# Kernel tuning notes

Hardware: AMD Instinct MI355X
Metric: run time of the kernel (lower is better)

The kernel has to match this reference:

```python
import jax, jax.numpy as jnp
import numpy as np

B, L, H, E, V = 32, 1024, 1024, 512, 8192

def setup_inputs() -> dict:
    key = jax.random.key(0)
    k1, k2, k3, k4 = jax.random.split(key, 4)
    x = jax.random.randint(k1, (B, L), 0, V)
    hidden = jnp.zeros((B, H), dtype=jnp.float32)  # equivalent to hidden=None path
    embedding = jax.random.normal(k2, (V, E), dtype=jnp.float32)
    W_h = jax.random.normal(k3, (E + H, H), dtype=jnp.float32) * 0.01
    b_h = jnp.zeros((H,), dtype=jnp.float32)
    W_o = jax.random.normal(k4, (H, V), dtype=jnp.float32) * 0.01
    b_o = jnp.zeros((V,), dtype=jnp.float32)
    return {"x": x, "hidden": hidden, "embedding": embedding,
            "W_h": W_h, "b_h": b_h, "W_o": W_o, "b_o": b_o}

def reference(x, hidden, embedding, W_h, b_h, W_o, b_o):
    # x: [B, L] int; hidden: [B, H]
    x_embed = embedding[x]                       # [B, L, E]
    x_tl = jnp.swapaxes(x_embed, 0, 1)           # [L, B, E] time-major

    def step(h, x_t):
        # concat + matmul + bias + tanh, one timestep
        combined = jnp.concatenate([x_t, h], axis=1)   # [B, E+H]
        h_new = jnp.tanh(combined @ W_h + b_h)         # [B, H]
        return h_new, h_new

    final_hidden, outs = jax.lax.scan(step, hidden, x_tl)  # outs: [L, B, H]
    output = jnp.swapaxes(outs, 0, 1)                       # [B, L, H]
    logits = output @ W_o + b_o                             # [B, L, V]
    return logits, final_hidden
```

## Files before the change

### kernel.cpp

```cpp
#include <hip/hip_runtime.h>
#include <hip/hip_bf16.h>

typedef unsigned short u16;
typedef unsigned int   u32;
typedef unsigned long long u64;
typedef __attribute__((ext_vector_type(8))) __bf16 bf16x8;
typedef __attribute__((ext_vector_type(4))) float   f32x4;

#define GLOAD16(gp, lp) __builtin_amdgcn_global_load_lds( \
    (__attribute__((address_space(1))) void*)(gp),        \
    (__attribute__((address_space(3))) void*)(lp), 16, 0, 0)

static __device__ __forceinline__ u16 f2bf(float f) {
  __bf16 b = (__bf16)f;
  return __builtin_bit_cast(u16, b);
}
static __device__ __forceinline__ f32x4 mfma16(bf16x8 a, bf16x8 b, f32x4 c) {
  return __builtin_amdgcn_mfma_f32_16x16x32_bf16(a, b, c, 0, 0, 0);
}


__global__ __launch_bounds__(256) void k_cvt_emb(const float* __restrict__ s,
                                                 u16* __restrict__ d) {
  int i = (blockIdx.x * 256 + threadIdx.x) * 4;
  float4 v = *(const float4*)(s + i);
  d[i] = f2bf(v.x); d[i+1] = f2bf(v.y); d[i+2] = f2bf(v.z); d[i+3] = f2bf(v.w);
}

__global__ __launch_bounds__(256) void k_tr_wh(const float* __restrict__ Wh,
                                               u16* __restrict__ WhxT,
                                               u16* __restrict__ WhhT) {
  __shared__ float tile[32][33];
  int bx = blockIdx.x & 31;
  int be = blockIdx.x >> 5;
  int tx = threadIdx.x & 31, ty = threadIdx.x >> 5;
  #pragma unroll
  for (int s = 0; s < 32; s += 8)
    tile[ty + s][tx] = Wh[(size_t)(be*32 + ty + s) * 1024 + bx*32 + tx];
  __syncthreads();
  #pragma unroll
  for (int s = 0; s < 32; s += 8) {
    int e = be*32 + tx;
    int j = bx*32 + ty + s;
    u16 v = f2bf(tile[tx][ty + s]);
    if (e < 512) WhxT[(size_t)j * 512 + e] = v;
    else         WhhT[(size_t)j * 1024 + (e - 512)] = v;
  }
}

__global__ __launch_bounds__(256) void k_tr_wo(const float* __restrict__ Wo,
                                               u16* __restrict__ WoT) {
  __shared__ float tile[32][33];
  int bx = blockIdx.x & 255;
  int by = blockIdx.x >> 8;
  int tx = threadIdx.x & 31, ty = threadIdx.x >> 5;
  #pragma unroll
  for (int s = 0; s < 32; s += 8)
    tile[ty + s][tx] = Wo[(size_t)(by*32 + ty + s) * 8192 + bx*32 + tx];
  __syncthreads();
  #pragma unroll
  for (int s = 0; s < 32; s += 8)
    WoT[(size_t)(bx*32 + ty + s) * 1024 + by*32 + tx] = f2bf(tile[tx][ty + s]);
}

__global__ __launch_bounds__(256) void k_init(const float* __restrict__ hid,
                                              u16* __restrict__ ring,
                                              unsigned* __restrict__ flags) {
  int i = blockIdx.x * 256 + threadIdx.x;
  ring[i] = f2bf(hid[i]);
  if (blockIdx.x < 8) flags[i] = 0;
}

__global__ __launch_bounds__(256) void k_xpart(const int* __restrict__ xq,
                                               const u16* __restrict__ embB,
                                               const u16* __restrict__ WhxT,
                                               const float* __restrict__ bh,
                                               float* __restrict__ xpart) {
  __shared__ __align__(16) u16 As[128 * 32];
  __shared__ __align__(16) u16 Bs[128 * 32];
  __shared__ int sx[128];
  int bid = blockIdx.x;
  int cpx = gridDim.x >> 3;
  int swz = (bid & 7) * cpx + (bid >> 3);
  int tm = (swz >> 3) * 128, tn = (swz & 7) * 128;
  int tid = threadIdx.x, lane = tid & 63, w = tid >> 6;
  int wm = (w >> 1) * 64, wn = (w & 1) * 64;
  if (tid < 128) sx[tid] = xq[tm + tid];
  __syncthreads();
  int r0 = tid >> 2, sub = tid & 3;
  const u16* ga0 = embB + (size_t)sx[r0] * 512 + sub * 8;
  const u16* ga1 = embB + (size_t)sx[64 + r0] * 512 + sub * 8;
  const u16* gb0 = WhxT + (size_t)(tn + r0) * 512 + sub * 8;
  const u16* gb1 = WhxT + (size_t)(tn + 64 + r0) * 512 + sub * 8;
  f32x4 acc[4][4] = {};
  int rl = lane & 15, kb = (lane >> 4) * 8;
  for (int kt = 0; kt < 16; ++kt) {
    int k0 = kt * 32;
    __syncthreads();
    GLOAD16(ga0 + k0, As + w * 512);
    GLOAD16(ga1 + k0, As + 2048 + w * 512);
    GLOAD16(gb0 + k0, Bs + w * 512);
    GLOAD16(gb1 + k0, Bs + 2048 + w * 512);
    __syncthreads();
    bf16x8 af[4], bf[4];
    #pragma unroll
    for (int mi = 0; mi < 4; mi++) af[mi] = *(const bf16x8*)&As[(wm + mi*16 + rl) * 32 + kb];
    #pragma unroll
    for (int ni = 0; ni < 4; ni++) bf[ni] = *(const bf16x8*)&Bs[(wn + ni*16 + rl) * 32 + kb];
    #pragma unroll
    for (int mi = 0; mi < 4; mi++)
      #pragma unroll
      for (int ni = 0; ni < 4; ni++)
        acc[mi][ni] = mfma16(af[mi], bf[ni], acc[mi][ni]);
  }
  int rq = (lane >> 4) << 2;
  #pragma unroll
  for (int ni = 0; ni < 4; ni++) {
    int col = tn + wn + ni*16 + rl;
    float bias = bh[col];
    #pragma unroll
    for (int mi = 0; mi < 4; mi++) {
      int row = tm + wm + mi*16 + rq;
      #pragma unroll
      for (int r = 0; r < 4; r++)
        xpart[(size_t)(row + r) * 1024 + col] = acc[mi][ni][r] + bias;
    }
  }
}

__global__ __launch_bounds__(256, 2) void k_fused(const u16* __restrict__ WhhT,
                                                  const float* __restrict__ xpart,
                                                  u16* __restrict__ ring,
                                                  float* __restrict__ hfinal,
                                                  unsigned* flags,
                                                  const u16* __restrict__ WoT,
                                                  const float* __restrict__ bo,
                                                  float* __restrict__ C) {
  __shared__ __align__(16) u16 smem[8192];
  __shared__ int sq;
  const int tid = threadIdx.x, lane = tid & 63, w = tid >> 6;

  if (blockIdx.x < 64) {
    float* psh = (float*)smem;
    int bid = blockIdx.x;
    int jbase = bid * 16;
    const int rl = lane & 15;
    const int kbase = w * 256 + ((lane >> 4) << 3);
    bf16x8 Wreg[8];
    #pragma unroll
    for (int ki = 0; ki < 8; ++ki)
      Wreg[ki] = *(const bf16x8*)&WhhT[(size_t)(jbase + rl) * 1024 + kbase + ki * 32];
    const bool red = (tid < 128);
    int b = 0, jq = 0, mi = 0, lsrc = 0, rg = 0;
    float4 xpre = make_float4(0.f, 0.f, 0.f, 0.f);
    if (red) {
      b = tid >> 2; jq = (tid & 3) << 2;
      mi = b >> 4;
      int bb = b & 15;
      lsrc = (bb >> 2) << 4;
      rg = bb & 3;
      xpre = *(const float4*)&xpart[(size_t)(b * 1024 + 0) * 1024 + jbase + jq];
    }
    for (int t = 0; t < 1024; ++t) {
      const u16* hprev = ring + (size_t)t * 32768;
      bf16x8 ha[16];
      #pragma unroll
      for (int ki = 0; ki < 8; ++ki) {
        int k = kbase + ki * 32;
        ha[ki*2 + 0] = *(const bf16x8*)&hprev[(size_t)rl * 1024 + k];
        ha[ki*2 + 1] = *(const bf16x8*)&hprev[(size_t)(16 + rl) * 1024 + k];
      }
      f32x4 acc0 = {0.f, 0.f, 0.f, 0.f}, acc1 = {0.f, 0.f, 0.f, 0.f};
      #pragma unroll
      for (int ki = 0; ki < 8; ++ki) {
        acc0 = mfma16(ha[ki*2 + 0], Wreg[ki], acc0);
        acc1 = mfma16(ha[ki*2 + 1], Wreg[ki], acc1);
      }
      *(f32x4*)&psh[((w * 2 + 0) * 64 + lane) * 4] = acc0;
      *(f32x4*)&psh[((w * 2 + 1) * 64 + lane) * 4] = acc1;
      __syncthreads();
      if (red) {
        float s0 = 0.f, s1 = 0.f, s2 = 0.f, s3 = 0.f;
        #pragma unroll
        for (int ww = 0; ww < 4; ++ww) {
          const float* pp = &psh[((ww * 2 + mi) * 64) * 4];
          s0 += pp[(lsrc + jq + 0) * 4 + rg];
          s1 += pp[(lsrc + jq + 1) * 4 + rg];
          s2 += pp[(lsrc + jq + 2) * 4 + rg];
          s3 += pp[(lsrc + jq + 3) * 4 + rg];
        }
        float v0 = tanhf(s0 + xpre.x);
        float v1 = tanhf(s1 + xpre.y);
        float v2 = tanhf(s2 + xpre.z);
        float v3 = tanhf(s3 + xpre.w);
        u32 lo = (u32)f2bf(v0) | ((u32)f2bf(v1) << 16);
        u32 hi = (u32)f2bf(v2) | ((u32)f2bf(v3) << 16);
        u64 hv = (u64)lo | ((u64)hi << 32);
        __hip_atomic_store((u64*)(ring + (size_t)(t + 1) * 32768 + b * 1024 + jbase + jq),
                           hv, __ATOMIC_RELAXED, __HIP_MEMORY_SCOPE_AGENT);
        if (t == 1023)
          *(float4*)&hfinal[b * 1024 + jbase + jq] = make_float4(v0, v1, v2, v3);
      }
      if (t < 1023) {
        asm volatile("s_waitcnt vmcnt(0)" ::: "memory");
        __syncthreads();
        if (tid == 0)
          __hip_atomic_store(&flags[bid * 32], (unsigned)(t + 1),
                             __ATOMIC_RELAXED, __HIP_MEMORY_SCOPE_AGENT);
        if (red)
          xpre = *(const float4*)&xpart[((size_t)(b * 1024 + (t + 1))) * 1024 + jbase + jq];
        if (w == 0) {
          while (__hip_atomic_load(&flags[lane * 32], __ATOMIC_RELAXED,
                                   __HIP_MEMORY_SCOPE_AGENT) < (unsigned)(t + 1)) { }
        }
        __syncthreads();
      } else {
        asm volatile("s_waitcnt vmcnt(0)" ::: "memory");
        __syncthreads();
        if (tid == 0)
          __hip_atomic_store(&flags[bid * 32], 1024u,
                             __ATOMIC_RELAXED, __HIP_MEMORY_SCOPE_AGENT);
      }
    }
    return;
  }

  u16* As = smem;
  u16* Bs = smem + 4096;
  unsigned* qctr = flags + 2047;
  const u16* A = ring + 32768;
  const int wm = (w >> 1) * 64, wn = (w & 1) * 64;
  const int r0 = tid >> 2, sub = tid & 3;
  const int rl = lane & 15, kb = (lane >> 4) * 8;
  const int rq = (lane >> 4) << 2;
  const unsigned* myflag = flags + (blockIdx.x & 63) * 32;
  for (;;) {
    if (tid == 0)
      sq = (int)__hip_atomic_fetch_add(qctr, 1u, __ATOMIC_RELAXED,
                                       __HIP_MEMORY_SCOPE_AGENT);
    __syncthreads();
    const int q = sq;
    if (q >= 16384) return;
    const int tIdx = q >> 6, vIdx = q & 63;
    const int tm = tIdx * 128, tn = vIdx * 128;
    if (tIdx < 255) {
      if (tid == 0) {
        unsigned tgt = (unsigned)(tIdx * 4 + 5);
        while (__hip_atomic_load(myflag, __ATOMIC_RELAXED,
                                 __HIP_MEMORY_SCOPE_AGENT) < tgt)
          __builtin_amdgcn_s_sleep(127);
      }
    } else {
      if (tid < 64) {
        const unsigned* fp = flags + tid * 32;
        for (;;) {
          unsigned v = __hip_atomic_load(fp, __ATOMIC_RELAXED, __HIP_MEMORY_SCOPE_AGENT);
          if (!__any((int)(v < 1024u))) break;
          __builtin_amdgcn_s_sleep(127);
        }
      }
    }
    __syncthreads();
    const u16* ga0 = A + (size_t)(tm + r0) * 1024 + sub * 8;
    const u16* ga1 = A + (size_t)(tm + 64 + r0) * 1024 + sub * 8;
    const u16* gb0 = WoT + (size_t)(tn + r0) * 1024 + sub * 8;
    const u16* gb1 = WoT + (size_t)(tn + 64 + r0) * 1024 + sub * 8;
    f32x4 acc[4][4] = {};
    for (int kt = 0; kt < 32; ++kt) {
      int k0 = kt * 32;
      __syncthreads();
      GLOAD16(ga0 + k0, As + w * 512);
      GLOAD16(ga1 + k0, As + 2048 + w * 512);
      GLOAD16(gb0 + k0, Bs + w * 512);
      GLOAD16(gb1 + k0, Bs + 2048 + w * 512);
      __syncthreads();
      bf16x8 af[4], bf[4];
      #pragma unroll
      for (int mi = 0; mi < 4; mi++) af[mi] = *(const bf16x8*)&As[(wm + mi*16 + rl) * 32 + kb];
      #pragma unroll
      for (int ni = 0; ni < 4; ni++) bf[ni] = *(const bf16x8*)&Bs[(wn + ni*16 + rl) * 32 + kb];
      #pragma unroll
      for (int mi = 0; mi < 4; mi++)
        #pragma unroll
        for (int ni = 0; ni < 4; ni++)
          acc[mi][ni] = mfma16(af[mi], bf[ni], acc[mi][ni]);
    }
    #pragma unroll
    for (int ni = 0; ni < 4; ni++) {
      int col = tn + wn + ni*16 + rl;
      float bias = bo[col];
      #pragma unroll
      for (int mi = 0; mi < 4; mi++) {
        int row = tm + wm + mi*16 + rq;
        #pragma unroll
        for (int r = 0; r < 4; r++) {
          int m = row + r;
          size_t orow = (size_t)(((m & 31) << 10) | (m >> 5));
          C[orow * 8192 + col] = acc[mi][ni][r] + bias;
        }
      }
    }
  }
}

extern "C" void kernel_launch(void* const* d_in, const int* in_sizes, int n_in,
                              void* d_out, int out_size, void* d_ws, size_t ws_size,
                              hipStream_t stream) {
  const int*   x   = (const int*)  d_in[0];
  const float* hid = (const float*)d_in[1];
  const float* emb = (const float*)d_in[2];
  const float* Wh  = (const float*)d_in[3];
  const float* bh  = (const float*)d_in[4];
  const float* Wo  = (const float*)d_in[5];
  const float* bo  = (const float*)d_in[6];
  float* logits = (float*)d_out;
  float* hfinal = logits + (size_t)32768 * 8192;

  char* ws = (char*)d_ws;
  size_t off = 0;
  auto alloc = [&](size_t bytes) {
    char* p = ws + off;
    off += (bytes + 255) & ~(size_t)255;
    return p;
  };
  u16*   embB  = (u16*)  alloc((size_t)8192 * 512 * 2);
  u16*   WhxT  = (u16*)  alloc((size_t)1024 * 512 * 2);
  u16*   WhhT  = (u16*)  alloc((size_t)1024 * 1024 * 2);
  u16*   WoT   = (u16*)  alloc((size_t)8192 * 1024 * 2);
  float* xpart = (float*)alloc((size_t)32768 * 1024 * 4);
  u16*   ring  = (u16*)  alloc((size_t)1025 * 32768 * 2);
  unsigned* flags = (unsigned*)alloc(8192);
  (void)ws_size; (void)in_sizes; (void)n_in; (void)out_size;

  k_cvt_emb<<<4096, 256, 0, stream>>>(emb, embB);
  k_tr_wh  <<<1536, 256, 0, stream>>>(Wh, WhxT, WhhT);
  k_tr_wo  <<<8192, 256, 0, stream>>>(Wo, WoT);
  k_init   <<<128,  256, 0, stream>>>(hid, ring, flags);
  k_xpart  <<<2048, 256, 0, stream>>>(x, embB, WhxT, bh, xpart);
  k_fused  <<<256,  256, 0, stream>>>(WhhT, xpart, ring, hfinal, flags,
                                      WoT, bo, logits);
}
```

Before: 4.471 ms.

## Replace all-to-all flag polling with atomic counter barrier and replicated epoch flags

Each recurrent block used to publish its own step flag, and wave 0 polled all 64 block flags every timestep. Now each block does one atomic fetch-add on a shared counter. The last arriver writes the step epoch to 8 replicated flag lines, and every block spins on one of them with a single thread. The GEMM consumer blocks also wait on a replicated epoch flag instead of per-block flags, with the readiness target adjusted. This trims polling traffic at the cost of serialising 64 atomics onto one counter line each step.

Result: no change. 4.515 ms (+1.0%).

```diff
diff --git a/kernel.cpp b/kernel.cpp
--- a/kernel.cpp
+++ b/kernel.cpp
@@ -146,6 +146,8 @@
     int jbase = bid * 16;
     const int rl = lane & 15;
     const int kbase = w * 256 + ((lane >> 4) << 3);
+    unsigned* cnt = flags;
+    unsigned* ep  = flags + 64 + (bid & 7) * 32;
     bf16x8 Wreg[8];
     #pragma unroll
     for (int ki = 0; ki < 8; ++ki)
@@ -201,25 +203,26 @@
         if (t == 1023)
           *(float4*)&hfinal[b * 1024 + jbase + jq] = make_float4(v0, v1, v2, v3);
       }
+      asm volatile("s_waitcnt vmcnt(0)" ::: "memory");
+      __syncthreads();
+      if (tid == 0) {
+        u32 old = __hip_atomic_fetch_add(cnt, 1u, __ATOMIC_RELAXED,
+                                         __HIP_MEMORY_SCOPE_AGENT);
+        if (old == (u32)(t * 64 + 63)) {
+          #pragma unroll
+          for (int r = 0; r < 8; ++r)
+            __hip_atomic_store(flags + 64 + r * 32, (u32)(t + 1),
+                               __ATOMIC_RELAXED, __HIP_MEMORY_SCOPE_AGENT);
+        }
+      }
       if (t < 1023) {
-        asm volatile("s_waitcnt vmcnt(0)" ::: "memory");
-        __syncthreads();
-        if (tid == 0)
-          __hip_atomic_store(&flags[bid * 32], (unsigned)(t + 1),
-                             __ATOMIC_RELAXED, __HIP_MEMORY_SCOPE_AGENT);
         if (red)
           xpre = *(const float4*)&xpart[((size_t)(b * 1024 + (t + 1))) * 1024 + jbase + jq];
-        if (w == 0) {
-          while (__hip_atomic_load(&flags[lane * 32], __ATOMIC_RELAXED,
-                                   __HIP_MEMORY_SCOPE_AGENT) < (unsigned)(t + 1)) { }
+        if (tid == 0) {
+          while (__hip_atomic_load(ep, __ATOMIC_RELAXED,
+                                   __HIP_MEMORY_SCOPE_AGENT) < (u32)(t + 1)) { }
         }
         __syncthreads();
-      } else {
-        asm volatile("s_waitcnt vmcnt(0)" ::: "memory");
-        __syncthreads();
-        if (tid == 0)
-          __hip_atomic_store(&flags[bid * 32], 1024u,
-                             __ATOMIC_RELAXED, __HIP_MEMORY_SCOPE_AGENT);
       }
     }
     return;
@@ -233,7 +236,7 @@
   const int r0 = tid >> 2, sub = tid & 3;
   const int rl = lane & 15, kb = (lane >> 4) * 8;
   const int rq = (lane >> 4) << 2;
-  const unsigned* myflag = flags + (blockIdx.x & 63) * 32;
+  const unsigned* ep = flags + 64 + (blockIdx.x & 7) * 32;
   for (;;) {
     if (tid == 0)
       sq = (int)__hip_atomic_fetch_add(qctr, 1u, __ATOMIC_RELAXED,
@@ -243,22 +246,11 @@
     if (q >= 16384) return;
     const int tIdx = q >> 6, vIdx = q & 63;
     const int tm = tIdx * 128, tn = vIdx * 128;
-    if (tIdx < 255) {
-      if (tid == 0) {
-        unsigned tgt = (unsigned)(tIdx * 4 + 5);
-        while (__hip_atomic_load(myflag, __ATOMIC_RELAXED,
-                                 __HIP_MEMORY_SCOPE_AGENT) < tgt)
-          __builtin_amdgcn_s_sleep(127);
-      }
-    } else {
-      if (tid < 64) {
-        const unsigned* fp = flags + tid * 32;
-        for (;;) {
-          unsigned v = __hip_atomic_load(fp, __ATOMIC_RELAXED, __HIP_MEMORY_SCOPE_AGENT);
-          if (!__any((int)(v < 1024u))) break;
-          __builtin_amdgcn_s_sleep(127);
-        }
-      }
+    if (tid == 0) {
+      unsigned tgt = (unsigned)(tIdx * 4 + 4);
+      while (__hip_atomic_load(ep, __ATOMIC_RELAXED,
+                               __HIP_MEMORY_SCOPE_AGENT) < tgt)
+        __builtin_amdgcn_s_sleep(127);
     }
     __syncthreads();
     const u16* ga0 = A + (size_t)(tm + r0) * 1024 + sub * 8;
```
